# Kernel tuning notes

Hardware: AMD Instinct MI355X
Metric: run time of the kernel (lower is better)

## Reference

```python
import jax, jax.numpy as jnp
import numpy as np

B, P, H, W = 64, 2, 512, 512

def setup_inputs() -> dict:
    key = jax.random.key(0)
    k1, k2 = jax.random.split(key)
    inp = jax.random.normal(k1, (B, P, H, W), dtype=jnp.float32)
    tgt = jax.random.uniform(k2, (B, P, H, W), dtype=jnp.float32)
    return {"input": inp, "target": tgt}


def reference(input, target):
    b, p, h, w = input.shape  # p == 2 required by the original loss
    # DSNT soft-argmax: softmax over flattened heatmap, expectation over grids
    sm = jax.nn.softmax(input.reshape(b, p, h * w), axis=-1).reshape(b, p, h, w)
    x_grid = (jnp.arange(1, w + 1, dtype=input.dtype)) / w  # [W]
    y_grid = (jnp.arange(1, h + 1, dtype=input.dtype)) / h  # [H]
    pred_x = jnp.einsum('bphw,w->bp', sm, x_grid)
    pred_y = jnp.einsum('bphw,h->bp', sm, y_grid)
    # ground-truth argmax coords (detached / non-differentiable)
    am = jnp.argmax(target.reshape(b, p, h * w), axis=-1)  # [B,P]
    true_x = ((am % w).astype(input.dtype) + 1.0) / w
    true_y = ((am // w).astype(input.dtype) + 1.0) / h
    # euclidean distance loss per (sample, point)
    ed = jnp.sqrt((true_x - pred_x) ** 2 + (true_y - pred_y) ** 2)  # [B,P]
    s = jnp.sum(ed)
    # vector between point 0 and point 1 (x, y) per sample
    pred_vec = jnp.stack([pred_x[:, 0] - pred_x[:, 1], pred_y[:, 0] - pred_y[:, 1]], axis=-1)  # [B,2]
    true_vec = jnp.stack([true_x[:, 0] - true_x[:, 1], true_y[:, 0] - true_y[:, 1]], axis=-1)  # [B,2]
    pred_dist = jnp.sqrt(jnp.sum(pred_vec ** 2, axis=-1))  # [B]
    true_dist = jnp.sqrt(jnp.sum(true_vec ** 2, axis=-1))  # [B]
    s = s + jnp.sum(jnp.sqrt((pred_dist - true_dist) ** 2))
    # NOTE: original applies cos() to the cosine similarity (faithful reproduction)
    dot = jnp.sum(pred_vec * true_vec, axis=-1)  # [B]
    cos_distance = 1.0 - jnp.cos(dot / (pred_dist * true_dist))
    s = s + jnp.sum(cos_distance)
    return jnp.reshape(s / b, (1,))
```

## Files before the change

### kernel.cpp

```cpp
#include <hip/hip_runtime.h>
#include <math.h>

#define HH 512
#define WW 512
#define BP 128
#define SEG 16
#define PLANE (HH * WW)
#define SEG_ELEMS (PLANE / SEG)
#define NPART (BP * SEG)


__global__ __launch_bounds__(256) void dsnt_partial(
    const float* __restrict__ inp, const float* __restrict__ tgt,
    float* __restrict__ wsf, int* __restrict__ wsi)
{
    const int blk  = blockIdx.x;
    const int pair = blk >> 4;
    const int seg  = blk & 15;
    const int tid  = threadIdx.x;

    const size_t base = (size_t)pair * PLANE + (size_t)seg * SEG_ELEMS;
    const float4* __restrict__ ip = (const float4*)(inp + base);
    const float4* __restrict__ tp = (const float4*)(tgt + base);

    const float inv = 1.0f / 512.0f;

    float s = 0.0f, sx = 0.0f, sy = 0.0f;
    float mv = -1.0f;
    int   mi = 0;

#pragma unroll
    for (int t = 0; t < 16; ++t) {
        const int vidx = t * 256 + tid;
        const float4 a = ip[vidx];
        const float4 bb = tp[vidx];
        const int f = seg * SEG_ELEMS + vidx * 4;
        const float yw  = (float)((f >> 9) + 1) * inv;
        const float xw0 = (float)((f & 511) + 1) * inv;

        const float e0 = expf(a.x);
        const float e1 = expf(a.y);
        const float e2 = expf(a.z);
        const float e3 = expf(a.w);
        const float es = e0 + e1 + e2 + e3;
        s  += es;
        sx += es * xw0 + inv * (e1 + 2.0f * e2 + 3.0f * e3);
        sy += es * yw;

        if (bb.x > mv) { mv = bb.x; mi = f; }
        if (bb.y > mv) { mv = bb.y; mi = f + 1; }
        if (bb.z > mv) { mv = bb.z; mi = f + 2; }
        if (bb.w > mv) { mv = bb.w; mi = f + 3; }
    }

#pragma unroll
    for (int off = 32; off > 0; off >>= 1) {
        s  += __shfl_down(s,  off, 64);
        sx += __shfl_down(sx, off, 64);
        sy += __shfl_down(sy, off, 64);
        const float ov = __shfl_down(mv, off, 64);
        const int   oi = __shfl_down(mi, off, 64);
        if (ov > mv || (ov == mv && oi < mi)) { mv = ov; mi = oi; }
    }

    __shared__ float rs[4], rsx[4], rsy[4], rmv[4];
    __shared__ int   rmi[4];
    const int lane = tid & 63, wid = tid >> 6;
    if (lane == 0) { rs[wid] = s; rsx[wid] = sx; rsy[wid] = sy; rmv[wid] = mv; rmi[wid] = mi; }
    __syncthreads();
    if (tid == 0) {
        float fs = rs[0], fsx = rsx[0], fsy = rsy[0], fmv = rmv[0];
        int fmi = rmi[0];
#pragma unroll
        for (int k = 1; k < 4; ++k) {
            fs += rs[k]; fsx += rsx[k]; fsy += rsy[k];
            if (rmv[k] > fmv || (rmv[k] == fmv && rmi[k] < fmi)) { fmv = rmv[k]; fmi = rmi[k]; }
        }
        wsf[blk]            = fs;
        wsf[NPART + blk]    = fsx;
        wsf[2 * NPART + blk] = fsy;
        wsf[3 * NPART + blk] = fmv;
        wsi[blk]            = fmi;
    }
}

__global__ __launch_bounds__(128) void dsnt_finalize(
    const float* __restrict__ wsf, const int* __restrict__ wsi,
    float* __restrict__ out)
{
    __shared__ float px[BP], py[BP], tx[BP], ty[BP];
    __shared__ float wsum[2];
    const int tid = threadIdx.x;

    {
        float s = 0.0f, sx = 0.0f, sy = 0.0f, mv = -1.0f;
        int mi = 0;
#pragma unroll
        for (int k = 0; k < SEG; ++k) {
            const int i = tid * SEG + k;
            s  += wsf[i];
            sx += wsf[NPART + i];
            sy += wsf[2 * NPART + i];
            const float v = wsf[3 * NPART + i];
            const int  ii = wsi[i];
            if (v > mv || (v == mv && ii < mi)) { mv = v; mi = ii; }
        }
        px[tid] = sx / s;
        py[tid] = sy / s;
        tx[tid] = (float)((mi & 511) + 1) * (1.0f / 512.0f);
        ty[tid] = (float)((mi >> 9) + 1) * (1.0f / 512.0f);
    }
    __syncthreads();

    float term = 0.0f;
    if (tid < 64) {
        const int b = tid;
        const float px0 = px[2 * b], px1 = px[2 * b + 1];
        const float py0 = py[2 * b], py1 = py[2 * b + 1];
        const float tx0 = tx[2 * b], tx1 = tx[2 * b + 1];
        const float ty0 = ty[2 * b], ty1 = ty[2 * b + 1];

        const float ed0 = sqrtf((tx0 - px0) * (tx0 - px0) + (ty0 - py0) * (ty0 - py0));
        const float ed1 = sqrtf((tx1 - px1) * (tx1 - px1) + (ty1 - py1) * (ty1 - py1));

        const float pvx = px0 - px1, pvy = py0 - py1;
        const float tvx = tx0 - tx1, tvy = ty0 - ty1;
        const float pd = sqrtf(pvx * pvx + pvy * pvy);
        const float td = sqrtf(tvx * tvx + tvy * tvy);
        const float dot = pvx * tvx + pvy * tvy;
        const float cosd = 1.0f - cosf(dot / (pd * td));
        term = ed0 + ed1 + fabsf(pd - td) + cosd;
    }

#pragma unroll
    for (int off = 32; off > 0; off >>= 1)
        term += __shfl_down(term, off, 64);
    const int lane = tid & 63, wid = tid >> 6;
    if (lane == 0) wsum[wid] = term;
    __syncthreads();
    if (tid == 0) out[0] = (wsum[0] + wsum[1]) * (1.0f / 64.0f);
}

extern "C" void kernel_launch(void* const* d_in, const int* in_sizes, int n_in,
                              void* d_out, int out_size, void* d_ws, size_t ws_size,
                              hipStream_t stream)
{
    const float* inp = (const float*)d_in[0];
    const float* tgt = (const float*)d_in[1];
    float* out = (float*)d_out;
    float* wsf = (float*)d_ws;
    int*   wsi = (int*)((float*)d_ws + 4 * NPART);

    dsnt_partial<<<NPART, 256, 0, stream>>>(inp, tgt, wsf, wsi);
    dsnt_finalize<<<1, 128, 0, stream>>>(wsf, wsi, out);
}
```

Baseline: 285.9 us.

## Split softmax and argmax into separate block sets with batched loads

The partial kernel now launches 8192 blocks of 128 threads. The first half computes softmax-weighted sums over the input and the second half computes argmax over the target, so each block streams a single tensor. Each thread issues all 16 float4 loads up front, with a sched_barrier to keep them ahead of the math, and uses __expf plus four independent argmax lanes to shorten dependency chains. The finalize kernel now reduces 32 partials per plane instead of 16, which adds workspace traffic, and the 16 float4s held per thread raise register pressure.

```diff
diff --git a/kernel.cpp b/kernel.cpp
--- a/kernel.cpp
+++ b/kernel.cpp
@@ -1,86 +1,144 @@
 #include <hip/hip_runtime.h>
 #include <math.h>
 
-#define HH 512
-#define WW 512
 #define BP 128
-#define SEG 16
-#define PLANE (HH * WW)
-#define SEG_ELEMS (PLANE / SEG)
-#define NPART (BP * SEG)
-
-
-__global__ __launch_bounds__(256) void dsnt_partial(
+#define PLANE 262144
+#define PLANE4 65536
+#define BLK_F4 2048
+#define NBLK 4096
+#define NPARTN 4096
+
+
+__global__ __launch_bounds__(128, 4) void dsnt_partial(
     const float* __restrict__ inp, const float* __restrict__ tgt,
     float* __restrict__ wsf, int* __restrict__ wsi)
 {
+    const int tid  = threadIdx.x;
     const int blk  = blockIdx.x;
-    const int pair = blk >> 4;
-    const int seg  = blk & 15;
-    const int tid  = threadIdx.x;
-
-    const size_t base = (size_t)pair * PLANE + (size_t)seg * SEG_ELEMS;
-    const float4* __restrict__ ip = (const float4*)(inp + base);
-    const float4* __restrict__ tp = (const float4*)(tgt + base);
-
+    const int lane = tid & 63, wid = tid >> 6;
     const float inv = 1.0f / 512.0f;
 
-    float s = 0.0f, sx = 0.0f, sy = 0.0f;
-    float mv = -1.0f;
-    int   mi = 0;
-
-#pragma unroll
-    for (int t = 0; t < 16; ++t) {
-        const int vidx = t * 256 + tid;
-        const float4 a = ip[vidx];
-        const float4 bb = tp[vidx];
-        const int f = seg * SEG_ELEMS + vidx * 4;
-        const float yw  = (float)((f >> 9) + 1) * inv;
-        const float xw0 = (float)((f & 511) + 1) * inv;
-
-        const float e0 = expf(a.x);
-        const float e1 = expf(a.y);
-        const float e2 = expf(a.z);
-        const float e3 = expf(a.w);
-        const float es = e0 + e1 + e2 + e3;
-        s  += es;
-        sx += es * xw0 + inv * (e1 + 2.0f * e2 + 3.0f * e3);
-        sy += es * yw;
-
-        if (bb.x > mv) { mv = bb.x; mi = f; }
-        if (bb.y > mv) { mv = bb.y; mi = f + 1; }
-        if (bb.z > mv) { mv = bb.z; mi = f + 2; }
-        if (bb.w > mv) { mv = bb.w; mi = f + 3; }
-    }
-
-#pragma unroll
-    for (int off = 32; off > 0; off >>= 1) {
-        s  += __shfl_down(s,  off, 64);
-        sx += __shfl_down(sx, off, 64);
-        sy += __shfl_down(sy, off, 64);
-        const float ov = __shfl_down(mv, off, 64);
-        const int   oi = __shfl_down(mi, off, 64);
-        if (ov > mv || (ov == mv && oi < mi)) { mv = ov; mi = oi; }
-    }
-
-    __shared__ float rs[4], rsx[4], rsy[4], rmv[4];
-    __shared__ int   rmi[4];
-    const int lane = tid & 63, wid = tid >> 6;
-    if (lane == 0) { rs[wid] = s; rsx[wid] = sx; rsy[wid] = sy; rmv[wid] = mv; rmi[wid] = mi; }
-    __syncthreads();
-    if (tid == 0) {
-        float fs = rs[0], fsx = rsx[0], fsy = rsy[0], fmv = rmv[0];
-        int fmi = rmi[0];
-#pragma unroll
-        for (int k = 1; k < 4; ++k) {
-            fs += rs[k]; fsx += rsx[k]; fsy += rsy[k];
-            if (rmv[k] > fmv || (rmv[k] == fmv && rmi[k] < fmi)) { fmv = rmv[k]; fmi = rmi[k]; }
-        }
-        wsf[blk]            = fs;
-        wsf[NPART + blk]    = fsx;
-        wsf[2 * NPART + blk] = fsy;
-        wsf[3 * NPART + blk] = fmv;
-        wsi[blk]            = fmi;
+    __shared__ float rs[2], rsx[2], rsy[2], rmv[2];
+    __shared__ int   rmi[2];
+
+    const int tin = wid * 1024 + lane;
+
+    if (blk < NBLK) {
+        const float4* __restrict__ bp = (const float4*)inp + (size_t)blk * BLK_F4;
+
+        const float4 v0  = bp[tin +  0 * 64];
+        const float4 v1  = bp[tin +  1 * 64];
+        const float4 v2  = bp[tin +  2 * 64];
+        const float4 v3  = bp[tin +  3 * 64];
+        const float4 v4  = bp[tin +  4 * 64];
+        const float4 v5  = bp[tin +  5 * 64];
+        const float4 v6  = bp[tin +  6 * 64];
+        const float4 v7  = bp[tin +  7 * 64];
+        const float4 v8  = bp[tin +  8 * 64];
+        const float4 v9  = bp[tin +  9 * 64];
+        const float4 v10 = bp[tin + 10 * 64];
+        const float4 v11 = bp[tin + 11 * 64];
+        const float4 v12 = bp[tin + 12 * 64];
+        const float4 v13 = bp[tin + 13 * 64];
+        const float4 v14 = bp[tin + 14 * 64];
+        const float4 v15 = bp[tin + 15 * 64];
+        __builtin_amdgcn_sched_barrier(0);
+
+        const int inplane4 = (blk & 31) * BLK_F4 + tin;
+        float s = 0.0f, sx = 0.0f, sy = 0.0f;
+
+#define SM_STEP(J, V)                                                     \
+        {                                                                 \
+            const int f = (inplane4 + (J) * 64) * 4;           \
+            const float yw  = (float)((f >> 9) + 1) * inv;                \
+            const float xw0 = (float)((f & 511) + 1) * inv;               \
+            const float e0 = __expf((V).x);                               \
+            const float e1 = __expf((V).y);                               \
+            const float e2 = __expf((V).z);                               \
+            const float e3 = __expf((V).w);                               \
+            const float es = e0 + e1 + e2 + e3;                           \
+            s  += es;                                                     \
+            sx += es * xw0 + inv * (e1 + 2.0f * e2 + 3.0f * e3);          \
+            sy += es * yw;                                                \
+        }
+        SM_STEP(0, v0)  SM_STEP(1, v1)  SM_STEP(2, v2)  SM_STEP(3, v3)
+        SM_STEP(4, v4)  SM_STEP(5, v5)  SM_STEP(6, v6)  SM_STEP(7, v7)
+        SM_STEP(8, v8)  SM_STEP(9, v9)  SM_STEP(10, v10) SM_STEP(11, v11)
+        SM_STEP(12, v12) SM_STEP(13, v13) SM_STEP(14, v14) SM_STEP(15, v15)
+#undef SM_STEP
+
+#pragma unroll
+        for (int off = 32; off > 0; off >>= 1) {
+            s  += __shfl_down(s,  off, 64);
+            sx += __shfl_down(sx, off, 64);
+            sy += __shfl_down(sy, off, 64);
+        }
+        if (lane == 0) { rs[wid] = s; rsx[wid] = sx; rsy[wid] = sy; }
+        __syncthreads();
+        if (tid == 0) {
+            wsf[blk]              = rs[0] + rs[1];
+            wsf[NPARTN + blk]     = rsx[0] + rsx[1];
+            wsf[2 * NPARTN + blk] = rsy[0] + rsy[1];
+        }
+    } else {
+        const int b2 = blk - NBLK;
+        const float4* __restrict__ bp = (const float4*)tgt + (size_t)b2 * BLK_F4;
+
+        const float4 t0  = bp[tin +  0 * 64];
+        const float4 t1  = bp[tin +  1 * 64];
+        const float4 t2  = bp[tin +  2 * 64];
+        const float4 t3  = bp[tin +  3 * 64];
+        const float4 t4  = bp[tin +  4 * 64];
+        const float4 t5  = bp[tin +  5 * 64];
+        const float4 t6  = bp[tin +  6 * 64];
+        const float4 t7  = bp[tin +  7 * 64];
+        const float4 t8  = bp[tin +  8 * 64];
+        const float4 t9  = bp[tin +  9 * 64];
+        const float4 t10 = bp[tin + 10 * 64];
+        const float4 t11 = bp[tin + 11 * 64];
+        const float4 t12 = bp[tin + 12 * 64];
+        const float4 t13 = bp[tin + 13 * 64];
+        const float4 t14 = bp[tin + 14 * 64];
+        const float4 t15 = bp[tin + 15 * 64];
+        __builtin_amdgcn_sched_barrier(0);
+
+        const int inplane4 = (b2 & 31) * BLK_F4 + tin;
+        float mvx = -1.0f, mvy = -1.0f, mvz = -1.0f, mvw = -1.0f;
+        int   mix = 0, miy = 1, miz = 2, miw = 3;
+
+#define AM_STEP(J, V)                                                     \
+        {                                                                 \
+            const int f = (inplane4 + (J) * 64) * 4;                      \
+            if ((V).x > mvx) { mvx = (V).x; mix = f; }                    \
+            if ((V).y > mvy) { mvy = (V).y; miy = f + 1; }                \
+            if ((V).z > mvz) { mvz = (V).z; miz = f + 2; }                \
+            if ((V).w > mvw) { mvw = (V).w; miw = f + 3; }                \
+        }
+        AM_STEP(0, t0)  AM_STEP(1, t1)  AM_STEP(2, t2)  AM_STEP(3, t3)
+        AM_STEP(4, t4)  AM_STEP(5, t5)  AM_STEP(6, t6)  AM_STEP(7, t7)
+        AM_STEP(8, t8)  AM_STEP(9, t9)  AM_STEP(10, t10) AM_STEP(11, t11)
+        AM_STEP(12, t12) AM_STEP(13, t13) AM_STEP(14, t14) AM_STEP(15, t15)
+#undef AM_STEP
+
+        float mv = mvx; int mi = mix;
+        if (mvy > mv || (mvy == mv && miy < mi)) { mv = mvy; mi = miy; }
+        if (mvz > mv || (mvz == mv && miz < mi)) { mv = mvz; mi = miz; }
+        if (mvw > mv || (mvw == mv && miw < mi)) { mv = mvw; mi = miw; }
+
+#pragma unroll
+        for (int off = 32; off > 0; off >>= 1) {
+            const float ov = __shfl_down(mv, off, 64);
+            const int   oi = __shfl_down(mi, off, 64);
+            if (ov > mv || (ov == mv && oi < mi)) { mv = ov; mi = oi; }
+        }
+        if (lane == 0) { rmv[wid] = mv; rmi[wid] = mi; }
+        __syncthreads();
+        if (tid == 0) {
+            float fmv = rmv[0]; int fmi = rmi[0];
+            if (rmv[1] > fmv || (rmv[1] == fmv && rmi[1] < fmi)) { fmv = rmv[1]; fmi = rmi[1]; }
+            wsf[3 * NPARTN + b2] = fmv;
+            wsi[b2]              = fmi;
+        }
     }
 }
 
@@ -91,17 +149,18 @@
     __shared__ float px[BP], py[BP], tx[BP], ty[BP];
     __shared__ float wsum[2];
     const int tid = threadIdx.x;
+    const int SPP = NPARTN / BP;
 
     {
         float s = 0.0f, sx = 0.0f, sy = 0.0f, mv = -1.0f;
         int mi = 0;
 #pragma unroll
-        for (int k = 0; k < SEG; ++k) {
-            const int i = tid * SEG + k;
+        for (int k = 0; k < SPP; ++k) {
+            const int i = tid * SPP + k;
             s  += wsf[i];
-            sx += wsf[NPART + i];
-            sy += wsf[2 * NPART + i];
-            const float v = wsf[3 * NPART + i];
+            sx += wsf[NPARTN + i];
+            sy += wsf[2 * NPARTN + i];
+            const float v = wsf[3 * NPARTN + i];
             const int  ii = wsi[i];
             if (v > mv || (v == mv && ii < mi)) { mv = v; mi = ii; }
         }
@@ -149,8 +208,8 @@
     const float* tgt = (const float*)d_in[1];
     float* out = (float*)d_out;
     float* wsf = (float*)d_ws;
-    int*   wsi = (int*)((float*)d_ws + 4 * NPART);
-
-    dsnt_partial<<<NPART, 256, 0, stream>>>(inp, tgt, wsf, wsi);
+    int*   wsi = (int*)((float*)d_ws + 4 * NPARTN);
+
+    dsnt_partial<<<2 * NBLK, 128, 0, stream>>>(inp, tgt, wsf, wsi);
     dsnt_finalize<<<1, 128, 0, stream>>>(wsf, wsi, out);
 }
```

Measured after the change: 282.2 us. No clear change (-1.3%).
